# Kernel optimization log

Hardware: AMD Instinct MI355X
Metric: run time of the kernel (lower is better)

Reference implementation:

```python
import jax, jax.numpy as jnp
import numpy as np

V, D, N, K = 500000, 64, 50000, 32


def setup_inputs() -> dict:
    key = jax.random.key(0)
    ks = jax.random.split(key, 8)
    return {
        "embeddings": jax.random.normal(ks[0], (V, D), dtype=jnp.float32),
        "W1": jax.random.normal(ks[1], (2 * D, D), dtype=jnp.float32) * 0.05,
        "b1": jnp.zeros((D,), dtype=jnp.float32),
        "W2": jax.random.normal(ks[2], (D, D), dtype=jnp.float32) * 0.05,
        "b2": jnp.zeros((D,), dtype=jnp.float32),
        "w3": jax.random.normal(ks[3], (D, 1), dtype=jnp.float32) * 0.05,
        "b3": jnp.zeros((1,), dtype=jnp.float32),
        "video_nodes": jax.random.randint(ks[4], (N,), 0, V, dtype=jnp.int32),
        "neigh_idx": jax.random.randint(ks[5], (N, K), 0, V, dtype=jnp.int32),
        "neigh_deg": jax.random.randint(ks[6], (N,), 0, K + 1, dtype=jnp.int32),
    }


def reference(embeddings, W1, b1, W2, b2, w3, b3, video_nodes, neigh_idx, neigh_deg):
    # Ragged neighbor gather (padded to K, masked by degree)
    e = embeddings[neigh_idx]                      # [N, K, D] neighbor embeddings
    u = embeddings[video_nodes]                    # [N, D]    center embeddings
    # GraphRec-style attention: MLP on [neigh, center] concat -> scalar score
    x = jnp.concatenate(
        [e, jnp.broadcast_to(u[:, None, :], e.shape)], axis=-1)  # [N, K, 2D]
    h = jax.nn.relu(x @ W1 + b1)
    h = jax.nn.relu(h @ W2 + b2)
    s = (h @ w3)[..., 0] + b3[0]                   # [N, K]
    mask = jnp.arange(K)[None, :] < neigh_deg[:, None]
    s = jnp.where(mask, s, -1e9)                   # mask padded neighbors
    att = jax.nn.softmax(s, axis=-1)               # softmax over valid neighbors
    out = jnp.einsum('nkd,nk->nd', e, att)         # attention-weighted sum
    # num_neighs == 0 -> fall back to node's own embedding
    out = jnp.where((neigh_deg > 0)[:, None], out, u)
    return out
```

## Files before the change

kernel.cpp:

```cpp
#include <hip/hip_runtime.h>
#include <hip/hip_bf16.h>

typedef __bf16 bf16x8 __attribute__((ext_vector_type(8)));
typedef float  f32x4  __attribute__((ext_vector_type(4)));

#define MFMA32(acc, a, b) acc = __builtin_amdgcn_mfma_f32_16x16x32_bf16(a, b, acc, 0, 0, 0)
#define LD4(p) (*(const float4*)(p))

__device__ __forceinline__ bf16x8 cvt8(float4 a, float4 b) {
  bf16x8 r;
  r[0] = (__bf16)a.x; r[1] = (__bf16)a.y; r[2] = (__bf16)a.z; r[3] = (__bf16)a.w;
  r[4] = (__bf16)b.x; r[5] = (__bf16)b.y; r[6] = (__bf16)b.z; r[7] = (__bf16)b.w;
  return r;
}

template <int CTRL>
__device__ __forceinline__ float dpp_mov(float x) {
  int yi = __builtin_amdgcn_update_dpp(0, __builtin_bit_cast(int, x), CTRL, 0xF, 0xF, true);
  return __builtin_bit_cast(float, yi);
}
template <int CTRL>
__device__ __forceinline__ float dpp_fadd(float x) { return x + dpp_mov<CTRL>(x); }
template <int CTRL>
__device__ __forceinline__ float dpp_fmax(float x) { return fmaxf(x, dpp_mov<CTRL>(x)); }

__global__ void prep_frags(const float* __restrict__ W1,
                           const float* __restrict__ W2,
                           __bf16* __restrict__ wf) {
  int idx = blockIdx.x * 256 + threadIdx.x;
  if (idx < 8192) {
    int j = idx & 7, lane = (idx >> 3) & 63, mt = (idx >> 9) & 3, ks = idx >> 11;
    int i = ks * 32 + ((lane >> 4) << 3) + j;
    int col = mt * 16 + (lane & 15);
    wf[idx] = (__bf16)W1[i * 64 + col];
  } else if (idx < 12288) {
    int t = idx - 8192;
    int j = t & 7, lane = (t >> 3) & 63, mt2 = (t >> 9) & 3, ks2 = (t >> 11) & 1;
    int g = (lane >> 4) & 3;
    int rho = (ks2 * 2 + (j >> 2)) * 16 + g * 4 + (j & 3);
    wf[idx] = (__bf16)W2[rho * 64 + mt2 * 16 + (lane & 15)];
  }
}

#define ISSUE_RAW(XN, XD, XI0, XI1) do {                                      \
    const float* up_ = emb + (long)(XN) * 64 + g * 8;                         \
    ru0 = LD4(up_); ru1 = LD4(up_ + 4); ru2 = LD4(up_ + 32); ru3 = LD4(up_ + 36); \
    const int a0_ = ((lr) < (XD)) ? (XI0) : (XN);                             \
    const float* p0_ = emb + (long)a0_ * 64 + g * 8;                          \
    re0a = LD4(p0_); re0b = LD4(p0_ + 4); re0c = LD4(p0_ + 32); re0d = LD4(p0_ + 36); \
    if ((XD) > 16) {                                                          \
      const int a1_ = (16 + (lr) < (XD)) ? (XI1) : (XN);                      \
      const float* p1_ = emb + (long)a1_ * 64 + g * 8;                        \
      re1a = LD4(p1_); re1b = LD4(p1_ + 4); re1c = LD4(p1_ + 32); re1d = LD4(p1_ + 36); \
    }                                                                         \
  } while (0)

__global__ __launch_bounds__(512) void graph_agg(
    const float* __restrict__ emb,
    const float* __restrict__ b1g,
    const float* __restrict__ b2g,
    const float* __restrict__ w3g,
    const float* __restrict__ b3g,
    const int* __restrict__ vn,
    const int* __restrict__ ni,
    const int* __restrict__ nd,
    const __bf16* __restrict__ wf,
    float* __restrict__ out,
    int N) {
  __shared__ __align__(16) unsigned char smem[25344];

  {
    const uint4* src = (const uint4*)wf;
    uint4* dst = (uint4*)smem;
#pragma unroll
    for (int i = 0; i < 3; i++) dst[threadIdx.x + i * 512] = src[threadIdx.x + i * 512];
    int t = threadIdx.x;
    if (t < 64) {
      ((float*)(smem + 24576))[t] = b1g[t];
      ((float*)(smem + 24832))[t] = b2g[t];
      ((float*)(smem + 25088))[t] = w3g[t];
    }
  }
  __syncthreads();

  const __bf16* w1f = (const __bf16*)smem;
  const __bf16* w2f = (const __bf16*)(smem + 16384);
  const int wid = threadIdx.x >> 6;
  const int l   = threadIdx.x & 63;
  const int g   = l >> 4;
  const int lr  = l & 15;
  const float b3v = b3g[0];

  const int gw = blockIdx.x * 8 + wid;
  const int nwaves = gridDim.x * 8;

  const float4 z4 = make_float4(0.f, 0.f, 0.f, 0.f);
  float4 ru0 = z4, ru1 = z4, ru2 = z4, ru3 = z4;
  float4 re0a = z4, re0b = z4, re0c = z4, re0d = z4;
  float4 re1a = z4, re1b = z4, re1c = z4, re1d = z4;

  int n = gw;
  int cd = 0;
  if (n < N) {
    const int n0 = vn[n];
    cd = nd[n];
    const int j0 = ni[(long)n * 32 + lr];
    const int j1 = ni[(long)n * 32 + 16 + lr];
    ISSUE_RAW(n0, cd, j0, j1);
  }

  for (; n < N; n += nwaves) {
    const bool m1 = (cd > 16);

    int nn = n + nwaves; if (nn >= N) nn = n;
    const int xn = vn[nn], xd = nd[nn];
    const int xi0 = ni[(long)nn * 32 + lr];
    const int xi1 = ni[(long)nn * 32 + 16 + lr];

    int boff = 24576;
    asm volatile("" : "+v"(boff));
    const unsigned char* bb = smem + boff;

    if (cd == 0) {
      if (lr == 0) {
        float* op = out + (long)n * 64;
        *(float4*)(op + g * 8)      = ru0;
        *(float4*)(op + g * 8 + 4)  = ru1;
        *(float4*)(op + 32 + g * 8) = ru2;
        *(float4*)(op + 36 + g * 8) = ru3;
      }
      ISSUE_RAW(xn, xd, xi0, xi1);
    } else {
      const bool v0c = (lr < cd);
      const bool v1c = m1 && (16 + lr < cd);
      bf16x8 ef00, ef01, ef10, ef11, uf0, uf1;
      {
        float4 a = v0c ? re0a : z4, b = v0c ? re0b : z4;
        float4 c = v0c ? re0c : z4, d = v0c ? re0d : z4;
        ef00 = cvt8(a, b); ef01 = cvt8(c, d);
      }
      if (m1) {
        float4 a = v1c ? re1a : z4, b = v1c ? re1b : z4;
        float4 c = v1c ? re1c : z4, d = v1c ? re1d : z4;
        ef10 = cvt8(a, b); ef11 = cvt8(c, d);
      }
      uf0 = cvt8(ru0, ru1); uf1 = cvt8(ru2, ru3);

      f32x4 acc1[4][2];
#pragma unroll
      for (int mt = 0; mt < 4; mt++) {
        f32x4 bv = *(const f32x4*)(bb + (mt * 16 + g * 4) * 4);
        acc1[mt][0] = bv; acc1[mt][1] = bv;
      }
      const bf16x8 xb0s[4] = {ef00, ef01, uf0, uf1};
      const bf16x8 xb1s[4] = {ef10, ef11, uf0, uf1};
#pragma unroll
      for (int ks = 0; ks < 4; ks++) {
#pragma unroll
        for (int mt = 0; mt < 4; mt++) {
          bf16x8 wa = *(const bf16x8*)(w1f + ((ks * 4 + mt) * 64 + l) * 8);
          MFMA32(acc1[mt][0], wa, xb0s[ks]);
          if (m1) MFMA32(acc1[mt][1], wa, xb1s[ks]);
        }
      }

      bf16x8 hb[2][2];
#pragma unroll
      for (int ks2 = 0; ks2 < 2; ks2++) {
#pragma unroll
        for (int nt = 0; nt < 2; nt++) {
          if (nt == 0 || m1) {
            bf16x8 v;
#pragma unroll
            for (int j = 0; j < 8; j++) {
              const int mt = ks2 * 2 + (j >> 2), r = j & 3;
              v[j] = (__bf16)fmaxf(acc1[mt][nt][r], 0.f);
            }
            hb[ks2][nt] = v;
          }
        }
      }

      f32x4 acc2[4][2];
#pragma unroll
      for (int mt2 = 0; mt2 < 4; mt2++) {
        f32x4 bv = *(const f32x4*)(bb + 256 + (mt2 * 16 + g * 4) * 4);
        acc2[mt2][0] = bv; acc2[mt2][1] = bv;
      }
#pragma unroll
      for (int ks2 = 0; ks2 < 2; ks2++) {
#pragma unroll
        for (int mt2 = 0; mt2 < 4; mt2++) {
          bf16x8 wa = *(const bf16x8*)(w2f + ((ks2 * 4 + mt2) * 64 + l) * 8);
          MFMA32(acc2[mt2][0], wa, hb[ks2][0]);
          if (m1) MFMA32(acc2[mt2][1], wa, hb[ks2][1]);
        }
      }

      ISSUE_RAW(xn, xd, xi0, xi1);

      float sv0 = 0.f, sv1 = 0.f;
#pragma unroll
      for (int mt2 = 0; mt2 < 4; mt2++) {
        f32x4 wv = *(const f32x4*)(bb + 512 + (mt2 * 16 + g * 4) * 4);
#pragma unroll
        for (int r = 0; r < 4; r++) {
          sv0 += fmaxf(acc2[mt2][0][r], 0.f) * wv[r];
          if (m1) sv1 += fmaxf(acc2[mt2][1][r], 0.f) * wv[r];
        }
      }
      sv0 += __shfl_xor(sv0, 16); sv0 += __shfl_xor(sv0, 32);
      if (m1) { sv1 += __shfl_xor(sv1, 16); sv1 += __shfl_xor(sv1, 32); }

      const bool w0 = (lr < cd);
      const bool w1v = m1 && (16 + lr < cd);
      sv0 = w0 ? (sv0 + b3v) : -1e30f;
      sv1 = w1v ? (sv1 + b3v) : -1e30f;

      float mx = fmaxf(sv0, sv1);
      mx = dpp_fmax<0x128>(mx);
      mx = dpp_fmax<0x124>(mx);
      mx = dpp_fmax<0x122>(mx);
      mx = dpp_fmax<0x121>(mx);

      float p0 = w0 ? __expf(sv0 - mx) : 0.f;
      float p1 = w1v ? __expf(sv1 - mx) : 0.f;
      float sum = p0 + p1;
      sum = dpp_fadd<0x128>(sum);
      sum = dpp_fadd<0x124>(sum);
      sum = dpp_fadd<0x122>(sum);
      sum = dpp_fadd<0x121>(sum);
      const float inv = 1.f / sum;
      const float a0 = p0 * inv, a1 = p1 * inv;

      float o[16];
#pragma unroll
      for (int j = 0; j < 8; j++) {
        float v = a0 * (float)ef00[j];
        if (m1) v += a1 * (float)ef10[j];
        o[j] = v;
        float w = a0 * (float)ef01[j];
        if (m1) w += a1 * (float)ef11[j];
        o[8 + j] = w;
      }
      float q8[8];
#pragma unroll
      for (int t = 0; t < 8; t++) {
        const bool up = (lr & 8);
        float sel = up ? o[t + 8] : o[t];
        float oth = up ? o[t] : o[t + 8];
        q8[t] = sel + dpp_mov<0x128>(oth);
      }
      float q4[4];
#pragma unroll
      for (int t = 0; t < 4; t++) {
        const bool up = (lr & 4);
        float sel = up ? q8[t + 4] : q8[t];
        float oth = up ? q8[t] : q8[t + 4];
        q4[t] = sel + __shfl_xor(oth, 4);
      }
      float q2[2];
#pragma unroll
      for (int t = 0; t < 2; t++) {
        const bool up = (lr & 2);
        float sel = up ? q4[t + 2] : q4[t];
        float oth = up ? q4[t] : q4[t + 2];
        q2[t] = sel + dpp_mov<0x4E>(oth);
      }
      {
        const bool up = (lr & 1);
        float sel = up ? q2[1] : q2[0];
        float oth = up ? q2[0] : q2[1];
        float r = sel + dpp_mov<0xB1>(oth);
        out[(long)n * 64 + ((lr >> 3) << 5) + g * 8 + (lr & 7)] = r;
      }
    }

    cd = xd;
  }
}

extern "C" void kernel_launch(void* const* d_in, const int* in_sizes, int n_in,
                              void* d_out, int out_size, void* d_ws, size_t ws_size,
                              hipStream_t stream) {
  const float* emb = (const float*)d_in[0];
  const float* W1  = (const float*)d_in[1];
  const float* b1  = (const float*)d_in[2];
  const float* W2  = (const float*)d_in[3];
  const float* b2  = (const float*)d_in[4];
  const float* w3  = (const float*)d_in[5];
  const float* b3  = (const float*)d_in[6];
  const int* vn = (const int*)d_in[7];
  const int* ni = (const int*)d_in[8];
  const int* nd = (const int*)d_in[9];
  float* out = (float*)d_out;
  const int N = in_sizes[7];
  __bf16* wf = (__bf16*)d_ws;

  prep_frags<<<48, 256, 0, stream>>>(W1, W2, wf);
  graph_agg<<<1024, 512, 0, stream>>>(emb, b1, b2, w3, b3, vn, ni, nd, wf, out, N);
}
```

Before: 82.06 us.

## Partition nodes by degree and pack two short-degree nodes per wave

```diff
diff --git a/kernel.cpp b/kernel.cpp
--- a/kernel.cpp
+++ b/kernel.cpp
@@ -23,6 +23,37 @@
 __device__ __forceinline__ float dpp_fadd(float x) { return x + dpp_mov<CTRL>(x); }
 template <int CTRL>
 __device__ __forceinline__ float dpp_fmax(float x) { return fmaxf(x, dpp_mov<CTRL>(x)); }
+
+__device__ __forceinline__ float tree16(const float* o, int lr) {
+  float q8[8];
+#pragma unroll
+  for (int t = 0; t < 8; t++) {
+    const bool up = (lr & 8);
+    float sel = up ? o[t + 8] : o[t];
+    float oth = up ? o[t] : o[t + 8];
+    q8[t] = sel + dpp_mov<0x128>(oth);
+  }
+  float q4[4];
+#pragma unroll
+  for (int t = 0; t < 4; t++) {
+    const bool up = (lr & 4);
+    float sel = up ? q8[t + 4] : q8[t];
+    float oth = up ? q8[t] : q8[t + 4];
+    q4[t] = sel + __shfl_xor(oth, 4);
+  }
+  float q2[2];
+#pragma unroll
+  for (int t = 0; t < 2; t++) {
+    const bool up = (lr & 2);
+    float sel = up ? q4[t + 2] : q4[t];
+    float oth = up ? q4[t] : q4[t + 2];
+    q2[t] = sel + dpp_mov<0x4E>(oth);
+  }
+  const bool up = (lr & 1);
+  float sel = up ? q2[1] : q2[0];
+  float oth = up ? q2[0] : q2[1];
+  return sel + dpp_mov<0xB1>(oth);
+}
 
 __global__ void prep_frags(const float* __restrict__ W1,
                            const float* __restrict__ W2,
@@ -42,31 +73,35 @@
   }
 }
 
-#define ISSUE_RAW(XN, XD, XI0, XI1) do {                                      \
-    const float* up_ = emb + (long)(XN) * 64 + g * 8;                         \
-    ru0 = LD4(up_); ru1 = LD4(up_ + 4); ru2 = LD4(up_ + 32); ru3 = LD4(up_ + 36); \
-    const int a0_ = ((lr) < (XD)) ? (XI0) : (XN);                             \
-    const float* p0_ = emb + (long)a0_ * 64 + g * 8;                          \
-    re0a = LD4(p0_); re0b = LD4(p0_ + 4); re0c = LD4(p0_ + 32); re0d = LD4(p0_ + 36); \
-    if ((XD) > 16) {                                                          \
-      const int a1_ = (16 + (lr) < (XD)) ? (XI1) : (XN);                      \
-      const float* p1_ = emb + (long)a1_ * 64 + g * 8;                        \
-      re1a = LD4(p1_); re1b = LD4(p1_ + 4); re1c = LD4(p1_ + 32); re1d = LD4(p1_ + 36); \
-    }                                                                         \
-  } while (0)
+__global__ void partition(const int* __restrict__ nd, const int* __restrict__ vn,
+                          const float* __restrict__ emb, float* __restrict__ out,
+                          int* __restrict__ l0, int* __restrict__ l1,
+                          int* __restrict__ cnt, int N) {
+  int t = blockIdx.x * 256 + threadIdx.x;
+  if (t >= N) return;
+  int d = nd[t];
+  if (d == 0) {
+    const float4* s = (const float4*)(emb + (long)vn[t] * 64);
+    float4* dst = (float4*)(out + (long)t * 64);
+#pragma unroll
+    for (int i = 0; i < 16; i++) dst[i] = s[i];
+  } else if (d <= 16) {
+    l0[atomicAdd(&cnt[0], 1)] = t;
+  } else {
+    l1[atomicAdd(&cnt[1], 1)] = t;
+  }
+}
 
 __global__ __launch_bounds__(512) void graph_agg(
     const float* __restrict__ emb,
-    const float* __restrict__ b1g,
-    const float* __restrict__ b2g,
-    const float* __restrict__ w3g,
-    const float* __restrict__ b3g,
-    const int* __restrict__ vn,
-    const int* __restrict__ ni,
+    const float* __restrict__ b1g, const float* __restrict__ b2g,
+    const float* __restrict__ w3g, const float* __restrict__ b3g,
+    const int* __restrict__ vn, const int* __restrict__ ni,
     const int* __restrict__ nd,
     const __bf16* __restrict__ wf,
-    float* __restrict__ out,
-    int N) {
+    const int* __restrict__ l0, const int* __restrict__ l1,
+    const int* __restrict__ cnt,
+    float* __restrict__ out, int N) {
   __shared__ __align__(16) unsigned char smem[25344];
 
   {
@@ -91,193 +126,168 @@
   const int lr  = l & 15;
   const float b3v = b3g[0];
 
+  const int nP = cnt[0];
+  const int nS = cnt[1];
+  const int npair = (nP + 1) >> 1;
+  const int total = npair + nS;
+
   const int gw = blockIdx.x * 8 + wid;
-  const int nwaves = gridDim.x * 8;
-
-  const float4 z4 = make_float4(0.f, 0.f, 0.f, 0.f);
-  float4 ru0 = z4, ru1 = z4, ru2 = z4, ru3 = z4;
-  float4 re0a = z4, re0b = z4, re0c = z4, re0d = z4;
-  float4 re1a = z4, re1b = z4, re1c = z4, re1d = z4;
-
-  int n = gw;
-  int cd = 0;
-  if (n < N) {
-    const int n0 = vn[n];
-    cd = nd[n];
-    const int j0 = ni[(long)n * 32 + lr];
-    const int j1 = ni[(long)n * 32 + 16 + lr];
-    ISSUE_RAW(n0, cd, j0, j1);
-  }
-
-  for (; n < N; n += nwaves) {
-    const bool m1 = (cd > 16);
-
-    int nn = n + nwaves; if (nn >= N) nn = n;
-    const int xn = vn[nn], xd = nd[nn];
-    const int xi0 = ni[(long)nn * 32 + lr];
-    const int xi1 = ni[(long)nn * 32 + 16 + lr];
+  const int nwav = gridDim.x * 8;
+  int item = gw;
+  if (item >= total) return;
+
+#define LOADDESC(IT, O0_, O1_, C0_, C1_, D0_, D1_, J0_, J1_) do {            \
+    if ((IT) < npair) {                                                      \
+      int a_ = l0[2 * (IT)];                                                 \
+      int b_ = (2 * (IT) + 1 < nP) ? l0[2 * (IT) + 1] : a_;                  \
+      O0_ = a_; O1_ = b_; C0_ = vn[a_]; C1_ = vn[b_];                        \
+      D0_ = nd[a_]; D1_ = nd[b_];                                            \
+      J0_ = ni[(long)a_ * 32 + lr]; J1_ = ni[(long)b_ * 32 + lr];            \
+    } else {                                                                 \
+      int a_ = l1[(IT) - npair];                                             \
+      O0_ = a_; O1_ = a_; C0_ = vn[a_]; C1_ = C0_;                           \
+      D0_ = nd[a_]; D1_ = D0_;                                               \
+      J0_ = ni[(long)a_ * 32 + lr]; J1_ = ni[(long)a_ * 32 + 16 + lr];       \
+    } } while (0)
+
+  int O0, O1, C0, C1, D0, D1, J0, J1;
+  LOADDESC(item, O0, O1, C0, C1, D0, D1, J0, J1);
+
+  for (; item < total; item += nwav) {
+    const bool isPair = item < npair;
+
+    const int thr  = isPair ? lr : 16 + lr;
+    const int idx0 = (lr  < D0) ? J0 : C0;
+    const int idx1 = (thr < D1) ? J1 : C1;
+    const float* p0 = emb + (long)idx0 * 64 + g * 8;
+    const float* p1 = emb + (long)idx1 * 64 + g * 8;
+    const float* qa = emb + (long)C0 * 64 + g * 8;
+    const float* qb = emb + (long)C1 * 64 + g * 8;
+    float4 e0a = LD4(p0), e0b = LD4(p0 + 4), e0c = LD4(p0 + 32), e0d = LD4(p0 + 36);
+    float4 e1a = LD4(p1), e1b = LD4(p1 + 4), e1c = LD4(p1 + 32), e1d = LD4(p1 + 36);
+    float4 ua0 = LD4(qa), ua1 = LD4(qa + 4), ua2 = LD4(qa + 32), ua3 = LD4(qa + 36);
+    float4 ub0 = LD4(qb), ub1 = LD4(qb + 4), ub2 = LD4(qb + 32), ub3 = LD4(qb + 36);
+    bf16x8 ef00 = cvt8(e0a, e0b), ef01 = cvt8(e0c, e0d);
+    bf16x8 ef10 = cvt8(e1a, e1b), ef11 = cvt8(e1c, e1d);
+    bf16x8 ufa0 = cvt8(ua0, ua1), ufa1 = cvt8(ua2, ua3);
+    bf16x8 ufb0 = cvt8(ub0, ub1), ufb1 = cvt8(ub2, ub3);
 
     int boff = 24576;
     asm volatile("" : "+v"(boff));
     const unsigned char* bb = smem + boff;
 
-    if (cd == 0) {
-      if (lr == 0) {
-        float* op = out + (long)n * 64;
-        *(float4*)(op + g * 8)      = ru0;
-        *(float4*)(op + g * 8 + 4)  = ru1;
-        *(float4*)(op + 32 + g * 8) = ru2;
-        *(float4*)(op + 36 + g * 8) = ru3;
+    f32x4 acc1[4][2];
+#pragma unroll
+    for (int mt = 0; mt < 4; mt++) {
+      f32x4 bv = *(const f32x4*)(bb + (mt * 16 + g * 4) * 4);
+      acc1[mt][0] = bv; acc1[mt][1] = bv;
+    }
+    const bf16x8 xb0s[4] = {ef00, ef01, ufa0, ufa1};
+    const bf16x8 xb1s[4] = {ef10, ef11, ufb0, ufb1};
+#pragma unroll
+    for (int ks = 0; ks < 4; ks++) {
+#pragma unroll
+      for (int mt = 0; mt < 4; mt++) {
+        bf16x8 wa = *(const bf16x8*)(w1f + ((ks * 4 + mt) * 64 + l) * 8);
+        MFMA32(acc1[mt][0], wa, xb0s[ks]);
+        MFMA32(acc1[mt][1], wa, xb1s[ks]);
       }
-      ISSUE_RAW(xn, xd, xi0, xi1);
+    }
+
+    bf16x8 hb[2][2];
+#pragma unroll
+    for (int ks2 = 0; ks2 < 2; ks2++)
+#pragma unroll
+      for (int nt = 0; nt < 2; nt++) {
+        bf16x8 v;
+#pragma unroll
+        for (int j = 0; j < 8; j++) {
+          const int mt = ks2 * 2 + (j >> 2), r = j & 3;
+          v[j] = (__bf16)fmaxf(acc1[mt][nt][r], 0.f);
+        }
+        hb[ks2][nt] = v;
+      }
+
+    f32x4 acc2[4][2];
+#pragma unroll
+    for (int mt2 = 0; mt2 < 4; mt2++) {
+      f32x4 bv = *(const f32x4*)(bb + 256 + (mt2 * 16 + g * 4) * 4);
+      acc2[mt2][0] = bv; acc2[mt2][1] = bv;
+    }
+#pragma unroll
+    for (int ks2 = 0; ks2 < 2; ks2++)
+#pragma unroll
+      for (int mt2 = 0; mt2 < 4; mt2++) {
+        bf16x8 wa = *(const bf16x8*)(w2f + ((ks2 * 4 + mt2) * 64 + l) * 8);
+        MFMA32(acc2[mt2][0], wa, hb[ks2][0]);
+        MFMA32(acc2[mt2][1], wa, hb[ks2][1]);
+      }
+
+    int P0, P1, Q0, Q1, E0, E1, K0, K1;
+    {
+      int nit = item + nwav; if (nit >= total) nit = item;
+      LOADDESC(nit, P0, P1, Q0, Q1, E0, E1, K0, K1);
+    }
+
+    float sv0 = 0.f, sv1 = 0.f;
+#pragma unroll
+    for (int mt2 = 0; mt2 < 4; mt2++) {
+      f32x4 wv = *(const f32x4*)(bb + 512 + (mt2 * 16 + g * 4) * 4);
+#pragma unroll
+      for (int r = 0; r < 4; r++) {
+        sv0 += fmaxf(acc2[mt2][0][r], 0.f) * wv[r];
+        sv1 += fmaxf(acc2[mt2][1][r], 0.f) * wv[r];
+      }
+    }
+    sv0 += __shfl_xor(sv0, 16); sv0 += __shfl_xor(sv0, 32);
+    sv1 += __shfl_xor(sv1, 16); sv1 += __shfl_xor(sv1, 32);
+
+    const bool v0 = (lr  < D0);
+    const bool v1 = (thr < D1);
+    sv0 = v0 ? (sv0 + b3v) : -1e30f;
+    sv1 = v1 ? (sv1 + b3v) : -1e30f;
+
+    float mxA = sv0, mxB = sv1;
+    mxA = dpp_fmax<0x128>(mxA); mxB = dpp_fmax<0x128>(mxB);
+    mxA = dpp_fmax<0x124>(mxA); mxB = dpp_fmax<0x124>(mxB);
+    mxA = dpp_fmax<0x122>(mxA); mxB = dpp_fmax<0x122>(mxB);
+    mxA = dpp_fmax<0x121>(mxA); mxB = dpp_fmax<0x121>(mxB);
+    if (!isPair) { float mj = fmaxf(mxA, mxB); mxA = mj; mxB = mj; }
+
+    float pA = v0 ? __expf(sv0 - mxA) : 0.f;
+    float pB = v1 ? __expf(sv1 - mxB) : 0.f;
+    float sA = pA, sB = pB;
+    sA = dpp_fadd<0x128>(sA); sB = dpp_fadd<0x128>(sB);
+    sA = dpp_fadd<0x124>(sA); sB = dpp_fadd<0x124>(sB);
+    sA = dpp_fadd<0x122>(sA); sB = dpp_fadd<0x122>(sB);
+    sA = dpp_fadd<0x121>(sA); sB = dpp_fadd<0x121>(sB);
+    if (!isPair) { float sj = sA + sB; sA = sj; sB = sj; }
+    const float aA = pA / sA;
+    const float aB = pB / sB;
+
+    float oA[16], oB[16];
+#pragma unroll
+    for (int j = 0; j < 8; j++) {
+      oA[j]     = aA * (float)ef00[j];
+      oA[8 + j] = aA * (float)ef01[j];
+      oB[j]     = aB * (float)ef10[j];
+      oB[8 + j] = aB * (float)ef11[j];
+    }
+    const int dim = ((lr >> 3) << 5) + g * 8 + (lr & 7);
+    if (isPair) {
+      float rA = tree16(oA, lr);
+      float rB = tree16(oB, lr);
+      out[(long)O0 * 64 + dim] = rA;
+      out[(long)O1 * 64 + dim] = rB;
     } else {
-      const bool v0c = (lr < cd);
-      const bool v1c = m1 && (16 + lr < cd);
-      bf16x8 ef00, ef01, ef10, ef11, uf0, uf1;
-      {
-        float4 a = v0c ? re0a : z4, b = v0c ? re0b : z4;
-        float4 c = v0c ? re0c : z4, d = v0c ? re0d : z4;
-        ef00 = cvt8(a, b); ef01 = cvt8(c, d);
-      }
-      if (m1) {
-        float4 a = v1c ? re1a : z4, b = v1c ? re1b : z4;
-        float4 c = v1c ? re1c : z4, d = v1c ? re1d : z4;
-        ef10 = cvt8(a, b); ef11 = cvt8(c, d);
-      }
-      uf0 = cvt8(ru0, ru1); uf1 = cvt8(ru2, ru3);
-
-      f32x4 acc1[4][2];
-#pragma unroll
-      for (int mt = 0; mt < 4; mt++) {
-        f32x4 bv = *(const f32x4*)(bb + (mt * 16 + g * 4) * 4);
-        acc1[mt][0] = bv; acc1[mt][1] = bv;
-      }
-      const bf16x8 xb0s[4] = {ef00, ef01, uf0, uf1};
-      const bf16x8 xb1s[4] = {ef10, ef11, uf0, uf1};
-#pragma unroll
-      for (int ks = 0; ks < 4; ks++) {
-#pragma unroll
-        for (int mt = 0; mt < 4; mt++) {
-          bf16x8 wa = *(const bf16x8*)(w1f + ((ks * 4 + mt) * 64 + l) * 8);
-          MFMA32(acc1[mt][0], wa, xb0s[ks]);
-          if (m1) MFMA32(acc1[mt][1], wa, xb1s[ks]);
-        }
-      }
-
-      bf16x8 hb[2][2];
-#pragma unroll
-      for (int ks2 = 0; ks2 < 2; ks2++) {
-#pragma unroll
-        for (int nt = 0; nt < 2; nt++) {
-          if (nt == 0 || m1) {
-            bf16x8 v;
-#pragma unroll
-            for (int j = 0; j < 8; j++) {
-              const int mt = ks2 * 2 + (j >> 2), r = j & 3;
-              v[j] = (__bf16)fmaxf(acc1[mt][nt][r], 0.f);
-            }
-            hb[ks2][nt] = v;
-          }
-        }
-      }
-
-      f32x4 acc2[4][2];
-#pragma unroll
-      for (int mt2 = 0; mt2 < 4; mt2++) {
-        f32x4 bv = *(const f32x4*)(bb + 256 + (mt2 * 16 + g * 4) * 4);
-        acc2[mt2][0] = bv; acc2[mt2][1] = bv;
-      }
-#pragma unroll
-      for (int ks2 = 0; ks2 < 2; ks2++) {
-#pragma unroll
-        for (int mt2 = 0; mt2 < 4; mt2++) {
-          bf16x8 wa = *(const bf16x8*)(w2f + ((ks2 * 4 + mt2) * 64 + l) * 8);
-          MFMA32(acc2[mt2][0], wa, hb[ks2][0]);
-          if (m1) MFMA32(acc2[mt2][1], wa, hb[ks2][1]);
-        }
-      }
-
-      ISSUE_RAW(xn, xd, xi0, xi1);
-
-      float sv0 = 0.f, sv1 = 0.f;
-#pragma unroll
-      for (int mt2 = 0; mt2 < 4; mt2++) {
-        f32x4 wv = *(const f32x4*)(bb + 512 + (mt2 * 16 + g * 4) * 4);
-#pragma unroll
-        for (int r = 0; r < 4; r++) {
-          sv0 += fmaxf(acc2[mt2][0][r], 0.f) * wv[r];
-          if (m1) sv1 += fmaxf(acc2[mt2][1][r], 0.f) * wv[r];
-        }
-      }
-      sv0 += __shfl_xor(sv0, 16); sv0 += __shfl_xor(sv0, 32);
-      if (m1) { sv1 += __shfl_xor(sv1, 16); sv1 += __shfl_xor(sv1, 32); }
-
-      const bool w0 = (lr < cd);
-      const bool w1v = m1 && (16 + lr < cd);
-      sv0 = w0 ? (sv0 + b3v) : -1e30f;
-      sv1 = w1v ? (sv1 + b3v) : -1e30f;
-
-      float mx = fmaxf(sv0, sv1);
-      mx = dpp_fmax<0x128>(mx);
-      mx = dpp_fmax<0x124>(mx);
-      mx = dpp_fmax<0x122>(mx);
-      mx = dpp_fmax<0x121>(mx);
-
-      float p0 = w0 ? __expf(sv0 - mx) : 0.f;
-      float p1 = w1v ? __expf(sv1 - mx) : 0.f;
-      float sum = p0 + p1;
-      sum = dpp_fadd<0x128>(sum);
-      sum = dpp_fadd<0x124>(sum);
-      sum = dpp_fadd<0x122>(sum);
-      sum = dpp_fadd<0x121>(sum);
-      const float inv = 1.f / sum;
-      const float a0 = p0 * inv, a1 = p1 * inv;
-
-      float o[16];
-#pragma unroll
-      for (int j = 0; j < 8; j++) {
-        float v = a0 * (float)ef00[j];
-        if (m1) v += a1 * (float)ef10[j];
-        o[j] = v;
-        float w = a0 * (float)ef01[j];
-        if (m1) w += a1 * (float)ef11[j];
-        o[8 + j] = w;
-      }
-      float q8[8];
-#pragma unroll
-      for (int t = 0; t < 8; t++) {
-        const bool up = (lr & 8);
-        float sel = up ? o[t + 8] : o[t];
-        float oth = up ? o[t] : o[t + 8];
-        q8[t] = sel + dpp_mov<0x128>(oth);
-      }
-      float q4[4];
-#pragma unroll
-      for (int t = 0; t < 4; t++) {
-        const bool up = (lr & 4);
-        float sel = up ? q8[t + 4] : q8[t];
-        float oth = up ? q8[t] : q8[t + 4];
-        q4[t] = sel + __shfl_xor(oth, 4);
-      }
-      float q2[2];
-#pragma unroll
-      for (int t = 0; t < 2; t++) {
-        const bool up = (lr & 2);
-        float sel = up ? q4[t + 2] : q4[t];
-        float oth = up ? q4[t] : q4[t + 2];
-        q2[t] = sel + dpp_mov<0x4E>(oth);
-      }
-      {
-        const bool up = (lr & 1);
-        float sel = up ? q2[1] : q2[0];
-        float oth = up ? q2[0] : q2[1];
-        float r = sel + dpp_mov<0xB1>(oth);
-        out[(long)n * 64 + ((lr >> 3) << 5) + g * 8 + (lr & 7)] = r;
-      }
-    }
-
-    cd = xd;
-  }
+#pragma unroll
+      for (int t = 0; t < 16; t++) oA[t] += oB[t];
+      out[(long)O0 * 64 + dim] = tree16(oA, lr);
+    }
+
+    O0 = P0; O1 = P1; C0 = Q0; C1 = Q1; D0 = E0; D1 = E1; J0 = K0; J1 = K1;
+  }
+#undef LOADDESC
 }
 
 extern "C" void kernel_launch(void* const* d_in, const int* in_sizes, int n_in,
@@ -295,8 +305,16 @@
   const int* nd = (const int*)d_in[9];
   float* out = (float*)d_out;
   const int N = in_sizes[7];
-  __bf16* wf = (__bf16*)d_ws;
-
+
+  char* wsb = (char*)d_ws;
+  __bf16* wf = (__bf16*)wsb;
+  int* cnt = (int*)(wsb + 24576);
+  int* lst0 = (int*)(wsb + 24584);
+  int* lst1 = lst0 + N;
+
+  hipMemsetAsync(cnt, 0, 8, stream);
   prep_frags<<<48, 256, 0, stream>>>(W1, W2, wf);
-  graph_agg<<<1024, 512, 0, stream>>>(emb, b1, b2, w3, b3, vn, ni, nd, wf, out, N);
-}
+  partition<<<(N + 255) / 256, 256, 0, stream>>>(nd, vn, emb, out, lst0, lst1, cnt, N);
+  graph_agg<<<1024, 512, 0, stream>>>(emb, b1, b2, w3, b3, vn, ni, nd, wf,
+                                      lst0, lst1, cnt, out, N);
+}
```

Measured after the change: 92.87 us. +13.2%, slower.

## Precompute center-node half of first MLP layer per node in separate kernel

Applied to the files above, without the earlier changes.

```diff
diff --git a/kernel.cpp b/kernel.cpp
--- a/kernel.cpp
+++ b/kernel.cpp
@@ -24,17 +24,48 @@
 template <int CTRL>
 __device__ __forceinline__ float dpp_fmax(float x) { return fmaxf(x, dpp_mov<CTRL>(x)); }
 
+__device__ __forceinline__ float tree16(const float* o, int lr) {
+  float q8[8];
+#pragma unroll
+  for (int t = 0; t < 8; t++) {
+    const bool up = (lr & 8);
+    float sel = up ? o[t + 8] : o[t];
+    float oth = up ? o[t] : o[t + 8];
+    q8[t] = sel + dpp_mov<0x128>(oth);
+  }
+  float q4[4];
+#pragma unroll
+  for (int t = 0; t < 4; t++) {
+    const bool up = (lr & 4);
+    float sel = up ? q8[t + 4] : q8[t];
+    float oth = up ? q8[t] : q8[t + 4];
+    q4[t] = sel + __shfl_xor(oth, 4);
+  }
+  float q2[2];
+#pragma unroll
+  for (int t = 0; t < 2; t++) {
+    const bool up = (lr & 2);
+    float sel = up ? q4[t + 2] : q4[t];
+    float oth = up ? q4[t] : q4[t + 2];
+    q2[t] = sel + dpp_mov<0x4E>(oth);
+  }
+  const bool up = (lr & 1);
+  float sel = up ? q2[1] : q2[0];
+  float oth = up ? q2[0] : q2[1];
+  return sel + dpp_mov<0xB1>(oth);
+}
+
 __global__ void prep_frags(const float* __restrict__ W1,
                            const float* __restrict__ W2,
                            __bf16* __restrict__ wf) {
   int idx = blockIdx.x * 256 + threadIdx.x;
-  if (idx < 8192) {
-    int j = idx & 7, lane = (idx >> 3) & 63, mt = (idx >> 9) & 3, ks = idx >> 11;
+  if (idx < 4096) {
+    int j = idx & 7, lane = (idx >> 3) & 63, mt = (idx >> 9) & 3, ks = (idx >> 11) & 1;
     int i = ks * 32 + ((lane >> 4) << 3) + j;
     int col = mt * 16 + (lane & 15);
     wf[idx] = (__bf16)W1[i * 64 + col];
-  } else if (idx < 12288) {
-    int t = idx - 8192;
+  } else if (idx < 8192) {
+    int t = idx - 4096;
     int j = t & 7, lane = (t >> 3) & 63, mt2 = (t >> 9) & 3, ks2 = (t >> 11) & 1;
     int g = (lane >> 4) & 3;
     int rho = (ks2 * 2 + (j >> 2)) * 16 + g * 4 + (j & 3);
@@ -42,49 +73,49 @@
   }
 }
 
-#define ISSUE_RAW(XN, XD, XI0, XI1) do {                                      \
-    const float* up_ = emb + (long)(XN) * 64 + g * 8;                         \
-    ru0 = LD4(up_); ru1 = LD4(up_ + 4); ru2 = LD4(up_ + 32); ru3 = LD4(up_ + 36); \
-    const int a0_ = ((lr) < (XD)) ? (XI0) : (XN);                             \
-    const float* p0_ = emb + (long)a0_ * 64 + g * 8;                          \
-    re0a = LD4(p0_); re0b = LD4(p0_ + 4); re0c = LD4(p0_ + 32); re0d = LD4(p0_ + 36); \
-    if ((XD) > 16) {                                                          \
-      const int a1_ = (16 + (lr) < (XD)) ? (XI1) : (XN);                      \
-      const float* p1_ = emb + (long)a1_ * 64 + g * 8;                        \
-      re1a = LD4(p1_); re1b = LD4(p1_ + 4); re1c = LD4(p1_ + 32); re1d = LD4(p1_ + 36); \
-    }                                                                         \
-  } while (0)
+__global__ void prep_y(const float* __restrict__ emb, const float* __restrict__ W1,
+                       const float* __restrict__ b1, const int* __restrict__ vn,
+                       float* __restrict__ Y, int N) {
+  int t = blockIdx.x * 256 + threadIdx.x;
+  int n = t >> 6, d = t & 63;
+  if (n >= N) return;
+  const float* u = emb + (long)vn[n] * 64;
+  float acc = b1[d];
+#pragma unroll 4
+  for (int k4 = 0; k4 < 16; k4++) {
+    float4 uv = LD4(u + k4 * 4);
+    const float* w = W1 + (64 + k4 * 4) * 64 + d;
+    acc += uv.x * w[0] + uv.y * w[64] + uv.z * w[128] + uv.w * w[192];
+  }
+  Y[(long)n * 64 + d] = acc;
+}
 
 __global__ __launch_bounds__(512) void graph_agg(
     const float* __restrict__ emb,
-    const float* __restrict__ b1g,
-    const float* __restrict__ b2g,
-    const float* __restrict__ w3g,
+    const float* __restrict__ b2g, const float* __restrict__ w3g,
     const float* __restrict__ b3g,
-    const int* __restrict__ vn,
-    const int* __restrict__ ni,
+    const int* __restrict__ vn, const int* __restrict__ ni,
     const int* __restrict__ nd,
     const __bf16* __restrict__ wf,
-    float* __restrict__ out,
-    int N) {
-  __shared__ __align__(16) unsigned char smem[25344];
+    const float* __restrict__ Y,
+    float* __restrict__ out, int N) {
+  __shared__ __align__(16) unsigned char smem[16896];
 
   {
     const uint4* src = (const uint4*)wf;
     uint4* dst = (uint4*)smem;
 #pragma unroll
-    for (int i = 0; i < 3; i++) dst[threadIdx.x + i * 512] = src[threadIdx.x + i * 512];
+    for (int i = 0; i < 2; i++) dst[threadIdx.x + i * 512] = src[threadIdx.x + i * 512];
     int t = threadIdx.x;
     if (t < 64) {
-      ((float*)(smem + 24576))[t] = b1g[t];
-      ((float*)(smem + 24832))[t] = b2g[t];
-      ((float*)(smem + 25088))[t] = w3g[t];
+      ((float*)(smem + 16384))[t] = b2g[t];
+      ((float*)(smem + 16640))[t] = w3g[t];
     }
   }
   __syncthreads();
 
   const __bf16* w1f = (const __bf16*)smem;
-  const __bf16* w2f = (const __bf16*)(smem + 16384);
+  const __bf16* w2f = (const __bf16*)(smem + 8192);
   const int wid = threadIdx.x >> 6;
   const int l   = threadIdx.x & 63;
   const int g   = l >> 4;
@@ -94,189 +125,140 @@
   const int gw = blockIdx.x * 8 + wid;
   const int nwaves = gridDim.x * 8;
 
-  const float4 z4 = make_float4(0.f, 0.f, 0.f, 0.f);
-  float4 ru0 = z4, ru1 = z4, ru2 = z4, ru3 = z4;
-  float4 re0a = z4, re0b = z4, re0c = z4, re0d = z4;
-  float4 re1a = z4, re1b = z4, re1c = z4, re1d = z4;
-
   int n = gw;
-  int cd = 0;
+  int node = 0, deg = 0, i0 = 0, i1 = 0;
   if (n < N) {
-    const int n0 = vn[n];
-    cd = nd[n];
-    const int j0 = ni[(long)n * 32 + lr];
-    const int j1 = ni[(long)n * 32 + 16 + lr];
-    ISSUE_RAW(n0, cd, j0, j1);
+    node = vn[n]; deg = nd[n];
+    i0 = ni[(long)n * 32 + lr]; i1 = ni[(long)n * 32 + 16 + lr];
   }
 
   for (; n < N; n += nwaves) {
+    const int cn = node, cd = deg, ci0 = i0, ci1 = i1;
+    {
+      int nn = n + nwaves; if (nn >= N) nn = n;
+      node = vn[nn]; deg = nd[nn];
+      i0 = ni[(long)nn * 32 + lr]; i1 = ni[(long)nn * 32 + 16 + lr];
+    }
+
+    if (cd == 0) {
+      out[(long)n * 64 + l] = emb[(long)cn * 64 + l];
+      continue;
+    }
     const bool m1 = (cd > 16);
 
-    int nn = n + nwaves; if (nn >= N) nn = n;
-    const int xn = vn[nn], xd = nd[nn];
-    const int xi0 = ni[(long)nn * 32 + lr];
-    const int xi1 = ni[(long)nn * 32 + 16 + lr];
-
-    int boff = 24576;
+    int boff = 16384;
     asm volatile("" : "+v"(boff));
     const unsigned char* bb = smem + boff;
 
-    if (cd == 0) {
-      if (lr == 0) {
-        float* op = out + (long)n * 64;
-        *(float4*)(op + g * 8)      = ru0;
-        *(float4*)(op + g * 8 + 4)  = ru1;
-        *(float4*)(op + 32 + g * 8) = ru2;
-        *(float4*)(op + 36 + g * 8) = ru3;
-      }
-      ISSUE_RAW(xn, xd, xi0, xi1);
-    } else {
-      const bool v0c = (lr < cd);
-      const bool v1c = m1 && (16 + lr < cd);
-      bf16x8 ef00, ef01, ef10, ef11, uf0, uf1;
-      {
-        float4 a = v0c ? re0a : z4, b = v0c ? re0b : z4;
-        float4 c = v0c ? re0c : z4, d = v0c ? re0d : z4;
-        ef00 = cvt8(a, b); ef01 = cvt8(c, d);
-      }
-      if (m1) {
-        float4 a = v1c ? re1a : z4, b = v1c ? re1b : z4;
-        float4 c = v1c ? re1c : z4, d = v1c ? re1d : z4;
-        ef10 = cvt8(a, b); ef11 = cvt8(c, d);
-      }
-      uf0 = cvt8(ru0, ru1); uf1 = cvt8(ru2, ru3);
-
-      f32x4 acc1[4][2];
+    bf16x8 ef00, ef01, ef10, ef11;
+    {
+      const int a = (lr < cd) ? ci0 : cn;
+      const float* p = emb + (long)a * 64 + g * 8;
+      ef00 = cvt8(LD4(p), LD4(p + 4));
+      ef01 = cvt8(LD4(p + 32), LD4(p + 36));
+    }
+    if (m1) {
+      const int a = (16 + lr < cd) ? ci1 : cn;
+      const float* p = emb + (long)a * 64 + g * 8;
+      ef10 = cvt8(LD4(p), LD4(p + 4));
+      ef11 = cvt8(LD4(p + 32), LD4(p + 36));
+    }
+
+    f32x4 acc[4][2];
+    const float* yb = Y + (long)n * 64;
+#pragma unroll
+    for (int mt = 0; mt < 4; mt++) {
+      f32x4 yv = *(const f32x4*)(yb + mt * 16 + g * 4);
+      acc[mt][0] = yv; acc[mt][1] = yv;
+    }
+    const bf16x8 xb0s[2] = {ef00, ef01};
+    const bf16x8 xb1s[2] = {ef10, ef11};
+#pragma unroll
+    for (int ks = 0; ks < 2; ks++) {
 #pragma unroll
       for (int mt = 0; mt < 4; mt++) {
-        f32x4 bv = *(const f32x4*)(bb + (mt * 16 + g * 4) * 4);
-        acc1[mt][0] = bv; acc1[mt][1] = bv;
-      }
-      const bf16x8 xb0s[4] = {ef00, ef01, uf0, uf1};
-      const bf16x8 xb1s[4] = {ef10, ef11, uf0, uf1};
-#pragma unroll
-      for (int ks = 0; ks < 4; ks++) {
-#pragma unroll
-        for (int mt = 0; mt < 4; mt++) {
-          bf16x8 wa = *(const bf16x8*)(w1f + ((ks * 4 + mt) * 64 + l) * 8);
-          MFMA32(acc1[mt][0], wa, xb0s[ks]);
-          if (m1) MFMA32(acc1[mt][1], wa, xb1s[ks]);
+        bf16x8 wa = *(const bf16x8*)(w1f + ((ks * 4 + mt) * 64 + l) * 8);
+        MFMA32(acc[mt][0], wa, xb0s[ks]);
+        if (m1) MFMA32(acc[mt][1], wa, xb1s[ks]);
+      }
+    }
+
+    bf16x8 hb[2][2];
+#pragma unroll
+    for (int ks2 = 0; ks2 < 2; ks2++)
+#pragma unroll
+      for (int nt = 0; nt < 2; nt++) {
+        if (nt == 0 || m1) {
+          bf16x8 v;
+#pragma unroll
+          for (int j = 0; j < 8; j++) {
+            const int mt = ks2 * 2 + (j >> 2), r = j & 3;
+            v[j] = (__bf16)fmaxf(acc[mt][nt][r], 0.f);
+          }
+          hb[ks2][nt] = v;
         }
       }
 
-      bf16x8 hb[2][2];
-#pragma unroll
-      for (int ks2 = 0; ks2 < 2; ks2++) {
-#pragma unroll
-        for (int nt = 0; nt < 2; nt++) {
-          if (nt == 0 || m1) {
-            bf16x8 v;
-#pragma unroll
-            for (int j = 0; j < 8; j++) {
-              const int mt = ks2 * 2 + (j >> 2), r = j & 3;
-              v[j] = (__bf16)fmaxf(acc1[mt][nt][r], 0.f);
-            }
-            hb[ks2][nt] = v;
-          }
-        }
-      }
-
-      f32x4 acc2[4][2];
+#pragma unroll
+    for (int mt2 = 0; mt2 < 4; mt2++) {
+      f32x4 bv = *(const f32x4*)(bb + (mt2 * 16 + g * 4) * 4);
+      acc[mt2][0] = bv; acc[mt2][1] = bv;
+    }
+#pragma unroll
+    for (int ks2 = 0; ks2 < 2; ks2++)
 #pragma unroll
       for (int mt2 = 0; mt2 < 4; mt2++) {
-        f32x4 bv = *(const f32x4*)(bb + 256 + (mt2 * 16 + g * 4) * 4);
-        acc2[mt2][0] = bv; acc2[mt2][1] = bv;
-      }
-#pragma unroll
-      for (int ks2 = 0; ks2 < 2; ks2++) {
-#pragma unroll
-        for (int mt2 = 0; mt2 < 4; mt2++) {
-          bf16x8 wa = *(const bf16x8*)(w2f + ((ks2 * 4 + mt2) * 64 + l) * 8);
-          MFMA32(acc2[mt2][0], wa, hb[ks2][0]);
-          if (m1) MFMA32(acc2[mt2][1], wa, hb[ks2][1]);
-        }
-      }
-
-      ISSUE_RAW(xn, xd, xi0, xi1);
-
-      float sv0 = 0.f, sv1 = 0.f;
-#pragma unroll
-      for (int mt2 = 0; mt2 < 4; mt2++) {
-        f32x4 wv = *(const f32x4*)(bb + 512 + (mt2 * 16 + g * 4) * 4);
-#pragma unroll
-        for (int r = 0; r < 4; r++) {
-          sv0 += fmaxf(acc2[mt2][0][r], 0.f) * wv[r];
-          if (m1) sv1 += fmaxf(acc2[mt2][1][r], 0.f) * wv[r];
-        }
-      }
-      sv0 += __shfl_xor(sv0, 16); sv0 += __shfl_xor(sv0, 32);
-      if (m1) { sv1 += __shfl_xor(sv1, 16); sv1 += __shfl_xor(sv1, 32); }
-
-      const bool w0 = (lr < cd);
-      const bool w1v = m1 && (16 + lr < cd);
-      sv0 = w0 ? (sv0 + b3v) : -1e30f;
-      sv1 = w1v ? (sv1 + b3v) : -1e30f;
-
-      float mx = fmaxf(sv0, sv1);
-      mx = dpp_fmax<0x128>(mx);
-      mx = dpp_fmax<0x124>(mx);
-      mx = dpp_fmax<0x122>(mx);
-      mx = dpp_fmax<0x121>(mx);
-
-      float p0 = w0 ? __expf(sv0 - mx) : 0.f;
-      float p1 = w1v ? __expf(sv1 - mx) : 0.f;
-      float sum = p0 + p1;
-      sum = dpp_fadd<0x128>(sum);
-      sum = dpp_fadd<0x124>(sum);
-      sum = dpp_fadd<0x122>(sum);
-      sum = dpp_fadd<0x121>(sum);
-      const float inv = 1.f / sum;
-      const float a0 = p0 * inv, a1 = p1 * inv;
-
-      float o[16];
-#pragma unroll
-      for (int j = 0; j < 8; j++) {
-        float v = a0 * (float)ef00[j];
-        if (m1) v += a1 * (float)ef10[j];
-        o[j] = v;
-        float w = a0 * (float)ef01[j];
-        if (m1) w += a1 * (float)ef11[j];
-        o[8 + j] = w;
-      }
-      float q8[8];
-#pragma unroll
-      for (int t = 0; t < 8; t++) {
-        const bool up = (lr & 8);
-        float sel = up ? o[t + 8] : o[t];
-        float oth = up ? o[t] : o[t + 8];
-        q8[t] = sel + dpp_mov<0x128>(oth);
-      }
-      float q4[4];
-#pragma unroll
-      for (int t = 0; t < 4; t++) {
-        const bool up = (lr & 4);
-        float sel = up ? q8[t + 4] : q8[t];
-        float oth = up ? q8[t] : q8[t + 4];
-        q4[t] = sel + __shfl_xor(oth, 4);
-      }
-      float q2[2];
-#pragma unroll
-      for (int t = 0; t < 2; t++) {
-        const bool up = (lr & 2);
-        float sel = up ? q4[t + 2] : q4[t];
-        float oth = up ? q4[t] : q4[t + 2];
-        q2[t] = sel + dpp_mov<0x4E>(oth);
-      }
-      {
-        const bool up = (lr & 1);
-        float sel = up ? q2[1] : q2[0];
-        float oth = up ? q2[0] : q2[1];
-        float r = sel + dpp_mov<0xB1>(oth);
-        out[(long)n * 64 + ((lr >> 3) << 5) + g * 8 + (lr & 7)] = r;
-      }
-    }
-
-    cd = xd;
+        bf16x8 wa = *(const bf16x8*)(w2f + ((ks2 * 4 + mt2) * 64 + l) * 8);
+        MFMA32(acc[mt2][0], wa, hb[ks2][0]);
+        if (m1) MFMA32(acc[mt2][1], wa, hb[ks2][1]);
+      }
+
+    float sv0 = 0.f, sv1 = 0.f;
+#pragma unroll
+    for (int mt2 = 0; mt2 < 4; mt2++) {
+      f32x4 wv = *(const f32x4*)(bb + 256 + (mt2 * 16 + g * 4) * 4);
+#pragma unroll
+      for (int r = 0; r < 4; r++) {
+        sv0 += fmaxf(acc[mt2][0][r], 0.f) * wv[r];
+        if (m1) sv1 += fmaxf(acc[mt2][1][r], 0.f) * wv[r];
+      }
+    }
+    sv0 += __shfl_xor(sv0, 16); sv0 += __shfl_xor(sv0, 32);
+    if (m1) { sv1 += __shfl_xor(sv1, 16); sv1 += __shfl_xor(sv1, 32); }
+
+    const bool v0 = (lr < cd);
+    const bool v1 = m1 && (16 + lr < cd);
+    sv0 = v0 ? (sv0 + b3v) : -1e30f;
+    sv1 = v1 ? (sv1 + b3v) : -1e30f;
+
+    float mx = fmaxf(sv0, sv1);
+    mx = dpp_fmax<0x128>(mx);
+    mx = dpp_fmax<0x124>(mx);
+    mx = dpp_fmax<0x122>(mx);
+    mx = dpp_fmax<0x121>(mx);
+
+    float p0 = v0 ? __expf(sv0 - mx) : 0.f;
+    float p1 = v1 ? __expf(sv1 - mx) : 0.f;
+    float sum = p0 + p1;
+    sum = dpp_fadd<0x128>(sum);
+    sum = dpp_fadd<0x124>(sum);
+    sum = dpp_fadd<0x122>(sum);
+    sum = dpp_fadd<0x121>(sum);
+    const float inv = 1.f / sum;
+    const float a0 = p0 * inv, a1 = p1 * inv;
+
+    float o[16];
+#pragma unroll
+    for (int j = 0; j < 8; j++) {
+      float v = a0 * (float)ef00[j];
+      if (m1) v += a1 * (float)ef10[j];
+      o[j] = v;
+      float w = a0 * (float)ef01[j];
+      if (m1) w += a1 * (float)ef11[j];
+      o[8 + j] = w;
+    }
+    const int dim = ((lr >> 3) << 5) + g * 8 + (lr & 7);
+    out[(long)n * 64 + dim] = tree16(o, lr);
   }
 }
 
@@ -295,8 +277,13 @@
   const int* nd = (const int*)d_in[9];
   float* out = (float*)d_out;
   const int N = in_sizes[7];
-  __bf16* wf = (__bf16*)d_ws;
-
-  prep_frags<<<48, 256, 0, stream>>>(W1, W2, wf);
-  graph_agg<<<1024, 512, 0, stream>>>(emb, b1, b2, w3, b3, vn, ni, nd, wf, out, N);
-}
+
+  char* wsb = (char*)d_ws;
+  __bf16* wf = (__bf16*)wsb;
+  size_t needY = 16384 + (size_t)N * 64 * 4;
+  float* Yp = (ws_size >= needY) ? (float*)(wsb + 16384) : out;
+
+  prep_frags<<<32, 256, 0, stream>>>(W1, W2, wf);
+  prep_y<<<(N * 64 + 255) / 256, 256, 0, stream>>>(emb, W1, b1, vn, Yp, N);
+  graph_agg<<<1024, 512, 0, stream>>>(emb, b2, w3, b3, vn, ni, nd, wf, Yp, out, N);
+}
```

After: 117.3 us. 43.0% more time.
